# Optimization experiments

Measured on AMD Instinct MI355X. Metric: run time of the kernel, lower is better.

The kernel has to match this reference:

```python
import jax, jax.numpy as jnp
import numpy as np
from jax import lax

DN3D = ('NDHWC', 'DHWIO', 'NDHWC')


def _conv3d(x, w):
    return lax.conv_general_dilated(x, w, window_strides=(1, 1, 1),
                                    padding='VALID', dimension_numbers=DN3D)


def _cconv3d(xr, xi, wr, wi):
    # (xr + i xi) * (wr + i wi)
    yr = _conv3d(xr, wr) - _conv3d(xi, wi)
    yi = _conv3d(xr, wi) + _conv3d(xi, wr)
    return yr, yi


def _project(wr, wi, zero_mean):
    # zero-mean + bound-norm weight projection over (kD,kH,kW,Cin) per output filter
    ax = (0, 1, 2, 3)
    if zero_mean:
        wr = wr - jnp.mean(wr, ax, keepdims=True)
        wi = wi - jnp.mean(wi, ax, keepdims=True)
    norm = jnp.sqrt(jnp.sum(wr * wr + wi * wi, ax, keepdims=True))
    s = 1.0 / jnp.maximum(norm, 1.0)
    return wr * s, wi * s


def _sympad(x, pads):
    # pads: list of (lo, hi) per axis
    return jnp.pad(x, pads, mode='symmetric')


def setup_inputs() -> dict:
    key = jax.random.key(0)
    ks = jax.random.split(key, 6)
    B, T, Z, Y, X, C = 2, 8, 20, 64, 64, 2
    F1, F = 32, 32
    return {
        'xr': jax.random.normal(ks[0], (B, T, Z, Y, X, C), jnp.float32),
        'xi': jax.random.normal(ks[1], (B, T, Z, Y, X, C), jnp.float32),
        'wxyz_r': jax.random.normal(ks[2], (3, 3, 3, C, F1), jnp.float32) * 0.1,
        'wxyz_i': jax.random.normal(ks[3], (3, 3, 3, C, F1), jnp.float32) * 0.1,
        'wt_r': jax.random.normal(ks[4], (3, 1, 1, F1, F), jnp.float32) * 0.1,
        'wt_i': jax.random.normal(ks[5], (3, 1, 1, F1, F), jnp.float32) * 0.1,
    }


def reference(xr, xi, wxyz_r, wxyz_i, wt_r, wt_i):
    B, T, Z, Y, X, C = xr.shape
    kz, ky, kx = wxyz_r.shape[0], wxyz_r.shape[1], wxyz_r.shape[2]
    kt = wt_r.shape[0]
    F1 = wxyz_r.shape[-1]
    F = wt_r.shape[-1]

    # projected (zero-mean, bound-norm) complex kernels
    wsr, wsi = _project(wxyz_r, wxyz_i, zero_mean=True)
    wtr, wti = _project(wt_r, wt_i, zero_mean=False)

    # --- spatial 3D conv over (Z,Y,X): fold T into batch (== per-T-slice loop)
    sr = xr.reshape(B * T, Z, Y, X, C)
    si = xi.reshape(B * T, Z, Y, X, C)
    pads_sp = [(0, 0), (kz // 2, kz // 2), (ky // 2, ky // 2), (kx // 2, kx // 2), (0, 0)]
    sr = _sympad(sr, pads_sp)
    si = _sympad(si, pads_sp)
    spr, spi = _cconv3d(sr, si, wsr, wsi)          # [B*T, Z, Y, X, F1]
    spr = spr.reshape(B, T, Z, Y, X, F1)
    spi = spi.reshape(B, T, Z, Y, X, F1)

    # --- temporal conv (kt,1,1) over (T,Z,Y): fold X into batch (== per-X-slice loop)
    tr = spr.transpose(0, 4, 1, 2, 3, 5).reshape(B * X, T, Z, Y, F1)
    ti = spi.transpose(0, 4, 1, 2, 3, 5).reshape(B * X, T, Z, Y, F1)
    pads_t = [(0, 0), (kt // 2, kt // 2), (0, 0), (0, 0), (0, 0)]
    tr = _sympad(tr, pads_t)
    ti = _sympad(ti, pads_t)
    ytr, yti = _cconv3d(tr, ti, wtr, wti)          # [B*X, T, Z, Y, F]
    yr = ytr.reshape(B, X, T, Z, Y, F).transpose(0, 2, 3, 4, 1, 5)
    yi = yti.reshape(B, X, T, Z, Y, F).transpose(0, 2, 3, 4, 1, 5)
    return yr, yi
```

## Files before the change

kernel.cpp:

```cpp
#include <hip/hip_runtime.h>

#define B_ 2
#define T_ 8
#define Z_ 20
#define Y_ 64
#define X_ 64
#define C_ 2
#define F1_ 32
#define F_ 32

constexpr int NPTS = B_*T_*Z_*Y_*X_;
constexpr int ZYX  = Z_*Y_*X_;

constexpr int RING_STRIDE = 36;
constexpr int SLOT_DW     = 16*RING_STRIDE;
constexpr int HALO2       = 3*3*34;

using bf8   = __attribute__((ext_vector_type(8))) short;
using f32x4 = __attribute__((ext_vector_type(4))) float;

__device__ inline unsigned short f2bf(float x) {
    unsigned u = __builtin_bit_cast(unsigned, x);
    return (unsigned short)((u + 0x7fff + ((u >> 16) & 1)) >> 16);
}
__device__ inline unsigned pk(float a, float b) {
    return (unsigned)f2bf(a) | ((unsigned)f2bf(b) << 16);
}

__global__ __launch_bounds__(64) void project_kernel(
    const float* __restrict__ wxr, const float* __restrict__ wxi,
    const float* __restrict__ wtr, const float* __restrict__ wti,
    float* __restrict__ psr, float* __restrict__ psi,
    float* __restrict__ otr, float* __restrict__ oti)
{
    const int bid  = blockIdx.x;
    const int lane = threadIdx.x;

    if (bid < F1_) {
        const int f = bid;
        float er = 0.f, ei = 0.f;
        if (lane < 54) { er = wxr[lane*F1_ + f]; ei = wxi[lane*F1_ + f]; }
        float sr = er, si = ei;
        #pragma unroll
        for (int o = 32; o >= 1; o >>= 1) { sr += __shfl_xor(sr, o); si += __shfl_xor(si, o); }
        const float mr = sr * (1.f/54.f), mi = si * (1.f/54.f);
        const float dr = er - mr, di = ei - mi;
        float sq = (lane < 54) ? (dr*dr + di*di) : 0.f;
        #pragma unroll
        for (int o = 32; o >= 1; o >>= 1) sq += __shfl_xor(sq, o);
        const float s = 1.f / fmaxf(sqrtf(sq), 1.f);
        if (lane < 54) { psr[lane*F1_ + f] = dr*s; psi[lane*F1_ + f] = di*s; }
    } else {
        const int f = bid - F1_;
        float er[2], ei[2];
        float sq = 0.f;
        #pragma unroll
        for (int k = 0; k < 2; ++k) {
            const int e = lane + k*64;
            if (e < 96) { er[k] = wtr[e*F_ + f]; ei[k] = wti[e*F_ + f]; sq += er[k]*er[k] + ei[k]*ei[k]; }
            else        { er[k] = 0.f;  ei[k] = 0.f; }
        }
        #pragma unroll
        for (int o = 32; o >= 1; o >>= 1) sq += __shfl_xor(sq, o);
        const float s = 1.f / fmaxf(sqrtf(sq), 1.f);
        #pragma unroll
        for (int k = 0; k < 2; ++k) {
            const int e = lane + k*64;
            if (e < 96) { otr[e*F_ + f] = er[k]*s; oti[e*F_ + f] = ei[k]*s; }
        }
    }
}

__global__ __launch_bounds__(256) void pack_kernel(
    const float* __restrict__ psr, const float* __restrict__ psi,
    const float* __restrict__ ptr_, const float* __restrict__ pti,
    unsigned short* __restrict__ wsp, unsigned short* __restrict__ wp)
{
    const int g = blockIdx.x;
    if (g < 16) {
        for (int o = g*512 + threadIdx.x; o < (g+1)*512; o += 256) {
            const int j  = o & 7;
            const int l  = (o >> 3) & 63;
            const int gg = o >> 9;
            const int kb = gg & 3, ct = gg >> 2;
            const int k  = kb*32 + (l >> 4)*8 + j;
            const int n  = ct*16 + (l & 15);
            float v = 0.f;
            if (k < 108) {
                const int tap = k >> 2, q = k & 3, cin = q & 1, cp = q >> 1;
                const int f  = n & 31;
                const float wr = psr[(tap*2 + cin)*F1_ + f];
                const float wi = psi[(tap*2 + cin)*F1_ + f];
                v = (n < 32) ? (cp ? -wi : wr) : (cp ? wr : wi);
            }
            wsp[o] = f2bf(v);
        }
    } else {
        for (int o = (g-16)*512 + threadIdx.x; o < (g-15)*512; o += 256) {
            const int j  = o & 7;
            const int l  = (o >> 3) & 63;
            const int gg = o >> 9;
            const int kb = gg % 6, ct = gg / 6;
            const int k  = kb*32 + (l >> 4)*8 + j;
            const int n  = ct*16 + (l & 15);
            const int kt = k >> 6, f1 = (k >> 1) & 31, c = k & 1;
            const int f  = n & 31;
            const float wr = ptr_[(kt*F1_ + f1)*F_ + f];
            const float wi = pti[(kt*F1_ + f1)*F_ + f];
            const float v  = (n < 32) ? (c ? -wi : wr) : (c ? wr : wi);
            wp[o] = f2bf(v);
        }
    }
}

__global__ __launch_bounds__(256) void repack_kernel(
    const float* __restrict__ xr, const float* __restrict__ xi,
    uint2* __restrict__ xb)
{
    const int p = blockIdx.x*256 + threadIdx.x;
    const float2 vr = *reinterpret_cast<const float2*>(xr + (size_t)p*2);
    const float2 vi = *reinterpret_cast<const float2*>(xi + (size_t)p*2);
    uint2 v;
    v.x = (unsigned)f2bf(vr.x) | ((unsigned)f2bf(vr.y) << 16);
    v.y = (unsigned)f2bf(vi.x) | ((unsigned)f2bf(vi.y) << 16);
    xb[p] = v;
}

__global__ __launch_bounds__(256, 2) void fused_kernel(
    const uint2* __restrict__ xb,
    const unsigned short* __restrict__ wsp,
    const unsigned short* __restrict__ wp,
    float* __restrict__ yr, float* __restrict__ yi)
{
    __shared__ uint4 ring4[4*2*3*SLOT_DW/4];
    __shared__ uint2 slab[4][2][HALO2];
    unsigned* ring = reinterpret_cast<unsigned*>(ring4);

    const int tid  = threadIdx.x;
    const int lane = tid & 63;
    const int wid  = tid >> 6;
    const int lx   = lane & 15;
    const int lg   = lane >> 4;

    const int bq    = blockIdx.x;
    const int ypair = bq & 31;
    const int z     = (bq >> 5) % Z_;
    const int b     = bq / (32*Z_);
    const int y     = ypair*2 + (wid >> 1);
    const int x0    = (wid & 1) * 32;

    bf8 wsf[4][4];
    const bf8* w8 = reinterpret_cast<const bf8*>(wsp);
    #pragma unroll
    for (int ct = 0; ct < 4; ++ct)
        #pragma unroll
        for (int kb = 0; kb < 4; ++kb)
            wsf[ct][kb] = w8[(ct*4 + kb)*64 + lane];

    bf8 wtf[4][6];
    const bf8* wp8 = reinterpret_cast<const bf8*>(wp);
    #pragma unroll
    for (int ct = 0; ct < 4; ++ct)
        #pragma unroll
        for (int kb = 0; kb < 6; ++kb)
            wtf[ct][kb] = wp8[(ct*6 + kb)*64 + lane];

    int xoff[5];
    #pragma unroll
    for (int i = 0; i < 5; ++i) {
        int it = lane + i*64; if (it >= HALO2) it = HALO2-1;
        const int iz = it / 102;
        const int iy = (it / 34) % 3;
        const int ix = it % 34;
        int zz = z + iz - 1;  zz = zz < 0 ? 0 : (zz >= Z_ ? Z_-1 : zz);
        int yy = y + iy - 1;  yy = yy < 0 ? 0 : (yy >= Y_ ? Y_-1 : yy);
        int xx = x0 + ix - 1; xx = xx < 0 ? 0 : (xx >= X_ ? X_-1 : xx);
        xoff[i] = (zz*Y_ + yy)*X_ + xx;
    }

    int o8[4][2];
    #pragma unroll
    for (int kb = 0; kb < 4; ++kb)
        #pragma unroll
        for (int s = 0; s < 2; ++s) {
            int ta = kb*8 + lg*2 + s; if (ta > 26) ta = 26;
            const int dz = ta/9, dyx = ta - dz*9, dy = dyx/3, dx = dyx - dy*3;
            o8[kb][s] = (dz*3 + dy)*34 + dx + lx;
        }

    unsigned* myring  = ring + wid*(2*3*SLOT_DW);
    const int  rbase  = lx*RING_STRIDE + lg*4;
    const size_t orow = (((size_t)b*T_)*Z_ + z)*(size_t)(Y_*X_) + (size_t)y*X_ + x0 + lx;

    uint4 caLo, caHi, cbLo, cbHi;
    uint2 stmp[5];

    auto STAGE_ISSUE = [&](int t) {
        const uint2* xt = xb + (size_t)(b*T_ + t)*ZYX;
        #pragma unroll
        for (int i = 0; i < 4; ++i) stmp[i] = xt[xoff[i]];
        if (lane < HALO2 - 256) stmp[4] = xt[xoff[4]];
    };
    auto STAGE_WRITE = [&](int bufsel) {
        uint2* s = slab[wid][bufsel];
        #pragma unroll
        for (int i = 0; i < 4; ++i) s[lane + i*64] = stmp[i];
        if (lane < HALO2 - 256) s[lane + 256] = stmp[4];
    };

    auto SPATIAL = [&](int bufsel, int xadd, uint4& lo, uint4& hi) {
        const uint2* s = slab[wid][bufsel];
        bf8 af[4];
        #pragma unroll
        for (int kb = 0; kb < 4; ++kb) {
            const uint2 l2 = s[o8[kb][0] + xadd];
            const uint2 h2 = s[o8[kb][1] + xadd];
            af[kb] = __builtin_bit_cast(bf8, make_uint4(l2.x, l2.y, h2.x, h2.y));
        }
        f32x4 acc[4];
        #pragma unroll
        for (int ct = 0; ct < 4; ++ct) acc[ct] = (f32x4){0.f,0.f,0.f,0.f};
        __builtin_amdgcn_s_setprio(1);
        #pragma unroll
        for (int ct = 0; ct < 4; ++ct)
            #pragma unroll
            for (int kb = 0; kb < 4; ++kb)
                acc[ct] = __builtin_amdgcn_mfma_f32_16x16x32_bf16(
                              wsf[ct][kb], af[kb], acc[ct], 0, 0, 0);
        __builtin_amdgcn_s_setprio(0);
        lo = make_uint4(pk(acc[0][0],acc[2][0]), pk(acc[0][1],acc[2][1]),
                        pk(acc[0][2],acc[2][2]), pk(acc[0][3],acc[2][3]));
        hi = make_uint4(pk(acc[1][0],acc[3][0]), pk(acc[1][1],acc[3][1]),
                        pk(acc[1][2],acc[3][2]), pk(acc[1][3],acc[3][3]));
    };

    auto WRITE = [&](int tsel, int t, const uint4& lo, const uint4& hi) {
        unsigned* s = myring + tsel*(3*SLOT_DW) + (t % 3)*SLOT_DW + rbase;
        *reinterpret_cast<uint4*>(s)      = lo;
        *reinterpret_cast<uint4*>(s + 16) = hi;
    };

    auto EMIT = [&](int tsel, const uint4& clo, const uint4& chi,
                    int sa, int sb, int tout) {
        const unsigned* tb = myring + tsel*(3*SLOT_DW);
        const unsigned* pa = tb + (sa % 3)*SLOT_DW + rbase;
        const unsigned* pb = tb + (sb % 3)*SLOT_DW + rbase;
        bf8 fr[6];
        fr[0] = __builtin_bit_cast(bf8, *reinterpret_cast<const uint4*>(pa));
        fr[1] = __builtin_bit_cast(bf8, *reinterpret_cast<const uint4*>(pa + 16));
        fr[2] = __builtin_bit_cast(bf8, *reinterpret_cast<const uint4*>(pb));
        fr[3] = __builtin_bit_cast(bf8, *reinterpret_cast<const uint4*>(pb + 16));
        fr[4] = __builtin_bit_cast(bf8, clo);
        fr[5] = __builtin_bit_cast(bf8, chi);
        f32x4 acc[4];
        #pragma unroll
        for (int ct = 0; ct < 4; ++ct) acc[ct] = (f32x4){0.f,0.f,0.f,0.f};
        __builtin_amdgcn_s_setprio(1);
        #pragma unroll
        for (int ct = 0; ct < 4; ++ct)
            #pragma unroll
            for (int kb = 0; kb < 6; ++kb)
                acc[ct] = __builtin_amdgcn_mfma_f32_16x16x32_bf16(
                              wtf[ct][kb], fr[kb], acc[ct], 0, 0, 0);
        __builtin_amdgcn_s_setprio(0);
        const size_t p = orow + tsel*16 + (size_t)tout * ZYX;
        #pragma unroll
        for (int ct = 0; ct < 4; ++ct) {
            float* outp = (ct < 2) ? yr : yi;
            *reinterpret_cast<f32x4*>(outp + p*F_ + (ct & 1)*16 + lg*4) = acc[ct];
        }
    };

    STAGE_ISSUE(0);
    STAGE_WRITE(0);
    STAGE_ISSUE(1);
    SPATIAL(0, 0,  caLo, caHi);
    SPATIAL(0, 16, cbLo, cbHi);
    WRITE(0, 0, caLo, caHi);
    WRITE(1, 0, cbLo, cbHi);

    #pragma unroll 1
    for (int t = 1; t < T_; ++t) {
        STAGE_WRITE(t & 1);
        if (t < T_-1) STAGE_ISSUE(t+1);
        const int sa = t-2 < 0 ? 0 : t-2;
        SPATIAL(t & 1, 0,  caLo, caHi);
        SPATIAL(t & 1, 16, cbLo, cbHi);
        EMIT(0, caLo, caHi, sa, t-1, t-1);
        EMIT(1, cbLo, cbHi, sa, t-1, t-1);
        WRITE(0, t, caLo, caHi);
        WRITE(1, t, cbLo, cbHi);
    }
    EMIT(0, caLo, caHi, T_-2, T_-1, T_-1);
    EMIT(1, cbLo, cbHi, T_-2, T_-1, T_-1);
}

extern "C" void kernel_launch(void* const* d_in, const int* in_sizes, int n_in,
                              void* d_out, int out_size, void* d_ws, size_t ws_size,
                              hipStream_t stream)
{
    const float* xr  = (const float*)d_in[0];
    const float* xi  = (const float*)d_in[1];
    const float* wxr = (const float*)d_in[2];
    const float* wxi = (const float*)d_in[3];
    const float* wtr = (const float*)d_in[4];
    const float* wti = (const float*)d_in[5];

    float* ws   = (float*)d_ws;
    float* psr  = ws;
    float* psi  = ws + 2048;
    float* ptr_ = ws + 4096;
    float* pti  = ws + 8192;
    unsigned short* wsp = (unsigned short*)(ws + 12288);
    unsigned short* wp  = (unsigned short*)(ws + 16384);
    uint2* xb           = (uint2*)(ws + 32768);

    float* yr = (float*)d_out;
    float* yi = yr + (size_t)NPTS * F_;

    hipLaunchKernelGGL(project_kernel, dim3(64), dim3(64), 0, stream,
                       wxr, wxi, wtr, wti, psr, psi, ptr_, pti);
    hipLaunchKernelGGL(pack_kernel, dim3(40), dim3(256), 0, stream,
                       psr, psi, ptr_, pti, wsp, wp);
    hipLaunchKernelGGL(repack_kernel, dim3(NPTS/256), dim3(256), 0, stream,
                       xr, xi, xb);
    hipLaunchKernelGGL(fused_kernel, dim3(B_*Z_*(Y_/2)), dim3(256), 0, stream,
                       xb, wsp, wp, yr, yi);
}
```

Before: 91.33 us.

## Fold spatial and temporal complex kernels into one 3x3x3x3 combined weight

Precomputes the product of the spatial and temporal complex weights into a single 81-tap combined kernel. The fused kernel then runs one MFMA chain straight from a 3-slot ring of input time slabs, replacing the two-stage spatial-then-temporal pipeline and its bf16 intermediate ring in LDS. This drops the intermediate rounding and packing and the LDS ring traffic, but raises the K dimension to 11 k-blocks (44 MFMAs per tile instead of 16+24) and the register pressure from 44 weight fragments. It also changes numerics, since the intermediate is never rounded to bf16. Boundary handling in time uses clamp-to-edge reads, which match symmetric padding of width one.

Measured after the change: 120.3 us, median of 2. 1.32x slower.

```diff
diff --git a/kernel.cpp b/kernel.cpp
--- a/kernel.cpp
+++ b/kernel.cpp
@@ -12,9 +12,9 @@
 constexpr int NPTS = B_*T_*Z_*Y_*X_;
 constexpr int ZYX  = Z_*Y_*X_;
 
-constexpr int RING_STRIDE = 36;
-constexpr int SLOT_DW     = 16*RING_STRIDE;
-constexpr int HALO2       = 3*3*34;
+constexpr int HALO2   = 3*3*34;
+constexpr int NKB     = 11;
+constexpr int K_REAL  = 324;
 
 using bf8   = __attribute__((ext_vector_type(8))) short;
 using f32x4 = __attribute__((ext_vector_type(4))) float;
@@ -71,45 +71,36 @@
     }
 }
 
-__global__ __launch_bounds__(256) void pack_kernel(
+__global__ __launch_bounds__(256) void pack_comb_kernel(
     const float* __restrict__ psr, const float* __restrict__ psi,
     const float* __restrict__ ptr_, const float* __restrict__ pti,
-    unsigned short* __restrict__ wsp, unsigned short* __restrict__ wp)
-{
-    const int g = blockIdx.x;
-    if (g < 16) {
-        for (int o = g*512 + threadIdx.x; o < (g+1)*512; o += 256) {
-            const int j  = o & 7;
-            const int l  = (o >> 3) & 63;
-            const int gg = o >> 9;
-            const int kb = gg & 3, ct = gg >> 2;
-            const int k  = kb*32 + (l >> 4)*8 + j;
-            const int n  = ct*16 + (l & 15);
-            float v = 0.f;
-            if (k < 108) {
-                const int tap = k >> 2, q = k & 3, cin = q & 1, cp = q >> 1;
-                const int f  = n & 31;
-                const float wr = psr[(tap*2 + cin)*F1_ + f];
-                const float wi = psi[(tap*2 + cin)*F1_ + f];
-                v = (n < 32) ? (cp ? -wi : wr) : (cp ? wr : wi);
+    unsigned short* __restrict__ wc)
+{
+    for (int o = blockIdx.x*512 + threadIdx.x; o < blockIdx.x*512 + 512; o += 256) {
+        const int j  = o & 7;
+        const int l  = (o >> 3) & 63;
+        const int g  = o >> 9;
+        const int kb = g % NKB, ct = g / NKB;
+        const int k  = kb*32 + (l >> 4)*8 + j;
+        const int n  = ct*16 + (l & 15);
+        float v = 0.f;
+        if (k < K_REAL) {
+            const int tap4 = k >> 2, q = k & 3, cin = q & 1, cp = q >> 1;
+            const int kt = tap4 / 27, tap = tap4 % 27;
+            const int f  = n & 31;
+            float cr = 0.f, ci = 0.f;
+            const float* wsr = psr + (tap*2 + cin)*F1_;
+            const float* wsi = psi + (tap*2 + cin)*F1_;
+            #pragma unroll 8
+            for (int f1 = 0; f1 < F1_; ++f1) {
+                const float ar = wsr[f1],                    ai = wsi[f1];
+                const float br = ptr_[(kt*F1_ + f1)*F_ + f], bi = pti[(kt*F1_ + f1)*F_ + f];
+                cr += ar*br - ai*bi;
+                ci += ar*bi + ai*br;
             }
-            wsp[o] = f2bf(v);
-        }
-    } else {
-        for (int o = (g-16)*512 + threadIdx.x; o < (g-15)*512; o += 256) {
-            const int j  = o & 7;
-            const int l  = (o >> 3) & 63;
-            const int gg = o >> 9;
-            const int kb = gg % 6, ct = gg / 6;
-            const int k  = kb*32 + (l >> 4)*8 + j;
-            const int n  = ct*16 + (l & 15);
-            const int kt = k >> 6, f1 = (k >> 1) & 31, c = k & 1;
-            const int f  = n & 31;
-            const float wr = ptr_[(kt*F1_ + f1)*F_ + f];
-            const float wi = pti[(kt*F1_ + f1)*F_ + f];
-            const float v  = (n < 32) ? (c ? -wi : wr) : (c ? wr : wi);
-            wp[o] = f2bf(v);
-        }
+            v = (n < 32) ? (cp ? -ci : cr) : (cp ? cr : ci);
+        }
+        wc[o] = f2bf(v);
     }
 }
 
@@ -128,13 +119,10 @@
 
 __global__ __launch_bounds__(256, 2) void fused_kernel(
     const uint2* __restrict__ xb,
-    const unsigned short* __restrict__ wsp,
-    const unsigned short* __restrict__ wp,
+    const unsigned short* __restrict__ wc,
     float* __restrict__ yr, float* __restrict__ yi)
 {
-    __shared__ uint4 ring4[4*2*3*SLOT_DW/4];
-    __shared__ uint2 slab[4][2][HALO2];
-    unsigned* ring = reinterpret_cast<unsigned*>(ring4);
+    __shared__ uint2 slab[4][3*HALO2];
 
     const int tid  = threadIdx.x;
     const int lane = tid & 63;
@@ -149,21 +137,13 @@
     const int y     = ypair*2 + (wid >> 1);
     const int x0    = (wid & 1) * 32;
 
-    bf8 wsf[4][4];
-    const bf8* w8 = reinterpret_cast<const bf8*>(wsp);
+    bf8 wcf[4][NKB];
+    const bf8* w8 = reinterpret_cast<const bf8*>(wc);
     #pragma unroll
     for (int ct = 0; ct < 4; ++ct)
         #pragma unroll
-        for (int kb = 0; kb < 4; ++kb)
-            wsf[ct][kb] = w8[(ct*4 + kb)*64 + lane];
-
-    bf8 wtf[4][6];
-    const bf8* wp8 = reinterpret_cast<const bf8*>(wp);
-    #pragma unroll
-    for (int ct = 0; ct < 4; ++ct)
-        #pragma unroll
-        for (int kb = 0; kb < 6; ++kb)
-            wtf[ct][kb] = wp8[(ct*6 + kb)*64 + lane];
+        for (int kb = 0; kb < NKB; ++kb)
+            wcf[ct][kb] = w8[(ct*NKB + kb)*64 + lane];
 
     int xoff[5];
     #pragma unroll
@@ -178,92 +158,59 @@
         xoff[i] = (zz*Y_ + yy)*X_ + xx;
     }
 
-    int o8[4][2];
+    unsigned koff2[NKB];
     #pragma unroll
-    for (int kb = 0; kb < 4; ++kb)
+    for (int kb = 0; kb < NKB; ++kb) {
+        unsigned pair = 0;
         #pragma unroll
         for (int s = 0; s < 2; ++s) {
-            int ta = kb*8 + lg*2 + s; if (ta > 26) ta = 26;
-            const int dz = ta/9, dyx = ta - dz*9, dy = dyx/3, dx = dyx - dy*3;
-            o8[kb][s] = (dz*3 + dy)*34 + dx + lx;
-        }
-
-    unsigned* myring  = ring + wid*(2*3*SLOT_DW);
-    const int  rbase  = lx*RING_STRIDE + lg*4;
+            int t4 = kb*8 + lg*2 + s; if (t4 > 80) t4 = 80;
+            const int kt = t4/27, tap = t4 - kt*27;
+            const int dz = tap/9, dyx = tap - dz*9, dy = dyx/3, dx = dyx - dy*3;
+            const unsigned off = kt*HALO2 + (dz*3 + dy)*34 + dx + lx;
+            pair |= off << (16*s);
+        }
+        koff2[kb] = pair;
+    }
+
+    uint2* sl = slab[wid];
     const size_t orow = (((size_t)b*T_)*Z_ + z)*(size_t)(Y_*X_) + (size_t)y*X_ + x0 + lx;
 
-    uint4 caLo, caHi, cbLo, cbHi;
     uint2 stmp[5];
 
-    auto STAGE_ISSUE = [&](int t) {
-        const uint2* xt = xb + (size_t)(b*T_ + t)*ZYX;
+    auto STAGE_ISSUE = [&](int tau) {
+        const int tc = tau < 0 ? 0 : (tau >= T_ ? T_-1 : tau);
+        const uint2* xt = xb + (size_t)(b*T_ + tc)*ZYX;
         #pragma unroll
         for (int i = 0; i < 4; ++i) stmp[i] = xt[xoff[i]];
         if (lane < HALO2 - 256) stmp[4] = xt[xoff[4]];
     };
-    auto STAGE_WRITE = [&](int bufsel) {
-        uint2* s = slab[wid][bufsel];
+    auto STAGE_WRITE = [&](int slot) {
+        uint2* s = sl + slot*HALO2;
         #pragma unroll
         for (int i = 0; i < 4; ++i) s[lane + i*64] = stmp[i];
         if (lane < HALO2 - 256) s[lane + 256] = stmp[4];
     };
 
-    auto SPATIAL = [&](int bufsel, int xadd, uint4& lo, uint4& hi) {
-        const uint2* s = slab[wid][bufsel];
-        bf8 af[4];
-        #pragma unroll
-        for (int kb = 0; kb < 4; ++kb) {
-            const uint2 l2 = s[o8[kb][0] + xadd];
-            const uint2 h2 = s[o8[kb][1] + xadd];
-            af[kb] = __builtin_bit_cast(bf8, make_uint4(l2.x, l2.y, h2.x, h2.y));
-        }
+    auto COMPUTE = [&](int rot, int t, int xadd, int tsel) {
         f32x4 acc[4];
         #pragma unroll
         for (int ct = 0; ct < 4; ++ct) acc[ct] = (f32x4){0.f,0.f,0.f,0.f};
         __builtin_amdgcn_s_setprio(1);
         #pragma unroll
-        for (int ct = 0; ct < 4; ++ct)
+        for (int kb = 0; kb < NKB; ++kb) {
+            int oa = (int)(koff2[kb] & 0xffffu) + rot; if (oa >= 3*HALO2) oa -= 3*HALO2;
+            int ob = (int)(koff2[kb] >> 16)     + rot; if (ob >= 3*HALO2) ob -= 3*HALO2;
+            const uint2 a0 = sl[oa + xadd];
+            const uint2 a1 = sl[ob + xadd];
+            const bf8 af = __builtin_bit_cast(bf8, make_uint4(a0.x, a0.y, a1.x, a1.y));
             #pragma unroll
-            for (int kb = 0; kb < 4; ++kb)
+            for (int ct = 0; ct < 4; ++ct)
                 acc[ct] = __builtin_amdgcn_mfma_f32_16x16x32_bf16(
-                              wsf[ct][kb], af[kb], acc[ct], 0, 0, 0);
+                              wcf[ct][kb], af, acc[ct], 0, 0, 0);
+        }
         __builtin_amdgcn_s_setprio(0);
-        lo = make_uint4(pk(acc[0][0],acc[2][0]), pk(acc[0][1],acc[2][1]),
-                        pk(acc[0][2],acc[2][2]), pk(acc[0][3],acc[2][3]));
-        hi = make_uint4(pk(acc[1][0],acc[3][0]), pk(acc[1][1],acc[3][1]),
-                        pk(acc[1][2],acc[3][2]), pk(acc[1][3],acc[3][3]));
-    };
-
-    auto WRITE = [&](int tsel, int t, const uint4& lo, const uint4& hi) {
-        unsigned* s = myring + tsel*(3*SLOT_DW) + (t % 3)*SLOT_DW + rbase;
-        *reinterpret_cast<uint4*>(s)      = lo;
-        *reinterpret_cast<uint4*>(s + 16) = hi;
-    };
-
-    auto EMIT = [&](int tsel, const uint4& clo, const uint4& chi,
-                    int sa, int sb, int tout) {
-        const unsigned* tb = myring + tsel*(3*SLOT_DW);
-        const unsigned* pa = tb + (sa % 3)*SLOT_DW + rbase;
-        const unsigned* pb = tb + (sb % 3)*SLOT_DW + rbase;
-        bf8 fr[6];
-        fr[0] = __builtin_bit_cast(bf8, *reinterpret_cast<const uint4*>(pa));
-        fr[1] = __builtin_bit_cast(bf8, *reinterpret_cast<const uint4*>(pa + 16));
-        fr[2] = __builtin_bit_cast(bf8, *reinterpret_cast<const uint4*>(pb));
-        fr[3] = __builtin_bit_cast(bf8, *reinterpret_cast<const uint4*>(pb + 16));
-        fr[4] = __builtin_bit_cast(bf8, clo);
-        fr[5] = __builtin_bit_cast(bf8, chi);
-        f32x4 acc[4];
-        #pragma unroll
-        for (int ct = 0; ct < 4; ++ct) acc[ct] = (f32x4){0.f,0.f,0.f,0.f};
-        __builtin_amdgcn_s_setprio(1);
-        #pragma unroll
-        for (int ct = 0; ct < 4; ++ct)
-            #pragma unroll
-            for (int kb = 0; kb < 6; ++kb)
-                acc[ct] = __builtin_amdgcn_mfma_f32_16x16x32_bf16(
-                              wtf[ct][kb], fr[kb], acc[ct], 0, 0, 0);
-        __builtin_amdgcn_s_setprio(0);
-        const size_t p = orow + tsel*16 + (size_t)tout * ZYX;
+        const size_t p = orow + tsel*16 + (size_t)t * ZYX;
         #pragma unroll
         for (int ct = 0; ct < 4; ++ct) {
             float* outp = (ct < 2) ? yr : yi;
@@ -271,28 +218,18 @@
         }
     };
 
-    STAGE_ISSUE(0);
-    STAGE_WRITE(0);
+    STAGE_ISSUE(-1); STAGE_WRITE(2);
+    STAGE_ISSUE(0);  STAGE_WRITE(0);
     STAGE_ISSUE(1);
-    SPATIAL(0, 0,  caLo, caHi);
-    SPATIAL(0, 16, cbLo, cbHi);
-    WRITE(0, 0, caLo, caHi);
-    WRITE(1, 0, cbLo, cbHi);
 
     #pragma unroll 1
-    for (int t = 1; t < T_; ++t) {
-        STAGE_WRITE(t & 1);
-        if (t < T_-1) STAGE_ISSUE(t+1);
-        const int sa = t-2 < 0 ? 0 : t-2;
-        SPATIAL(t & 1, 0,  caLo, caHi);
-        SPATIAL(t & 1, 16, cbLo, cbHi);
-        EMIT(0, caLo, caHi, sa, t-1, t-1);
-        EMIT(1, cbLo, cbHi, sa, t-1, t-1);
-        WRITE(0, t, caLo, caHi);
-        WRITE(1, t, cbLo, cbHi);
-    }
-    EMIT(0, caLo, caHi, T_-2, T_-1, T_-1);
-    EMIT(1, cbLo, cbHi, T_-2, T_-1, T_-1);
+    for (int t = 0; t < T_; ++t) {
+        STAGE_WRITE((t+1) % 3);
+        if (t < T_-1) STAGE_ISSUE(t+2);
+        const int rot = ((t+2) % 3) * HALO2;
+        COMPUTE(rot, t, 0,  0);
+        COMPUTE(rot, t, 16, 1);
+    }
 }
 
 extern "C" void kernel_launch(void* const* d_in, const int* in_sizes, int n_in,
@@ -311,19 +248,18 @@
     float* psi  = ws + 2048;
     float* ptr_ = ws + 4096;
     float* pti  = ws + 8192;
-    unsigned short* wsp = (unsigned short*)(ws + 12288);
-    unsigned short* wp  = (unsigned short*)(ws + 16384);
-    uint2* xb           = (uint2*)(ws + 32768);
+    unsigned short* wc = (unsigned short*)(ws + 12288);
+    uint2* xb          = (uint2*)(ws + 32768);
 
     float* yr = (float*)d_out;
     float* yi = yr + (size_t)NPTS * F_;
 
     hipLaunchKernelGGL(project_kernel, dim3(64), dim3(64), 0, stream,
                        wxr, wxi, wtr, wti, psr, psi, ptr_, pti);
-    hipLaunchKernelGGL(pack_kernel, dim3(40), dim3(256), 0, stream,
-                       psr, psi, ptr_, pti, wsp, wp);
+    hipLaunchKernelGGL(pack_comb_kernel, dim3(44), dim3(256), 0, stream,
+                       psr, psi, ptr_, pti, wc);
     hipLaunchKernelGGL(repack_kernel, dim3(NPTS/256), dim3(256), 0, stream,
                        xr, xi, xb);
     hipLaunchKernelGGL(fused_kernel, dim3(B_*Z_*(Y_/2)), dim3(256), 0, stream,
-                       xb, wsp, wp, yr, yi);
-}
+                       xb, wc, yr, yi);
+}
```
